# Performance work log

Measured on AMD Instinct MI355X. Metric: run time of the kernel, lower is better.

Reference implementation:

```python
import jax, jax.numpy as jnp
import numpy as np

NEAR, FAR = 2.0, 6.0
N_SAMPLES = 64
L_PTS, L_DIR = 10, 4
INF_DELTA = 1e10


def posenc(x, L):
    # x: [..., 3] -> [..., 3 + 6*L] (identity + sin/cos at 2^l frequencies)
    freqs = 2.0 ** jnp.arange(L, dtype=x.dtype)              # [L]
    ang = x[..., None, :] * freqs[:, None]                   # [..., L, 3]
    enc = jnp.concatenate([jnp.sin(ang), jnp.cos(ang)], axis=-1)  # [..., L, 6]
    return jnp.concatenate([x, enc.reshape(x.shape[:-1] + (L * 6,))], axis=-1)


def setup_inputs() -> dict:
    key = jax.random.key(0)
    ks = jax.random.split(key, 12)
    R, D, DH = 4096, 256, 128
    PE_P, PE_D = 3 + 6 * L_PTS, 3 + 6 * L_DIR  # 63, 27

    def w(k, shape):
        fan_in = shape[0]
        return jax.random.normal(k, shape, dtype=jnp.float32) / np.sqrt(fan_in)

    return {
        "xyz": jax.random.normal(ks[0], (1, R, 3), dtype=jnp.float32),
        "viewdirs": jax.random.normal(ks[1], (1, R, 3), dtype=jnp.float32),
        "W1": w(ks[2], (PE_P, D)), "b1": jnp.zeros((D,), jnp.float32),
        "W2": w(ks[3], (D, D)),    "b2": jnp.zeros((D,), jnp.float32),
        "W3": w(ks[4], (D, D)),    "b3": jnp.zeros((D,), jnp.float32),
        "Wsig": w(ks[5], (D, 1)),  "bsig": jnp.zeros((1,), jnp.float32),
        "Wfeat": w(ks[6], (D, D)), "bfeat": jnp.zeros((D,), jnp.float32),
        "Wdir": w(ks[7], (D + PE_D, DH)), "bdir": jnp.zeros((DH,), jnp.float32),
        "Wrgb": w(ks[8], (DH, 3)), "brgb": jnp.zeros((3,), jnp.float32),
    }


def reference(xyz, viewdirs, W1, b1, W2, b2, W3, b3, Wsig, bsig,
              Wfeat, bfeat, Wdir, bdir, Wrgb, brgb):
    xyz = xyz[0]          # [R, 3] (batch dim squeezed as in render_coarse)
    vd = viewdirs[0]
    vd = vd / jnp.linalg.norm(vd, axis=-1, keepdims=True)
    R = xyz.shape[0]

    # Evenly spaced samples between near and far (perturb=0 -> deterministic)
    t = jnp.linspace(0.0, 1.0, N_SAMPLES, dtype=xyz.dtype)
    samples = NEAR * (1.0 - t) + FAR * t                     # [N]
    samples = jnp.broadcast_to(samples, (R, N_SAMPLES))      # [R, N]
    delta = jnp.concatenate(
        [samples[:, 1:] - samples[:, :-1],
         jnp.full((R, 1), INF_DELTA, dtype=samples.dtype)], axis=-1)  # [R, N]

    # Sample points along each ray
    pts = xyz[:, None, :] + samples[..., None] * vd[:, None, :]  # [R, N, 3]

    # NeRF MLP: positional-encoded points -> density + view-dep color
    pe = posenc(pts, L_PTS)                                   # [R, N, 63]
    de = posenc(vd, L_DIR)                                    # [R, 27]
    h = jax.nn.relu(pe @ W1 + b1)
    h = jax.nn.relu(h @ W2 + b2)
    h = jax.nn.relu(h @ W3 + b3)                              # [R, N, 256]
    density = (h @ Wsig + bsig)[..., 0]                       # [R, N]
    feat = h @ Wfeat + bfeat                                  # [R, N, 256]
    de_b = jnp.broadcast_to(de[:, None, :], (R, N_SAMPLES, de.shape[-1]))
    hd = jax.nn.relu(jnp.concatenate([feat, de_b], axis=-1) @ Wdir + bdir)
    rgb = jax.nn.sigmoid(hd @ Wrgb + brgb)                    # [R, N, 3]

    # Volume rendering (alpha compositing with cumprod transmittance)
    sigma = jax.nn.relu(density)
    alpha = 1.0 - jnp.exp(-sigma * delta)                     # [R, N]
    T = jnp.concatenate(
        [jnp.ones((R, 1), alpha.dtype),
         jnp.cumprod(1.0 - alpha[:, :-1], axis=-1)], axis=-1)
    w = T * alpha                                             # [R, N]
    rgb_map = jnp.sum(w[..., None] * rgb, axis=-2)            # [R, 3]
    alpha_map = jnp.sum(w, axis=-1, keepdims=True)            # [R, 1]
    rgb_map = rgb_map + (1.0 - alpha_map)                     # white_bkgd
    depth_map = jnp.sum(w * samples, axis=-1)                 # [R]
    return rgb_map, depth_map, alpha_map
```

## Files before the change

kernel.cpp:

```cpp
#include <hip/hip_runtime.h>
#include <hip/hip_bf16.h>
#include <math.h>


typedef unsigned short u16;
typedef unsigned int   u32;
typedef __bf16 bf16x8 __attribute__((ext_vector_type(8)));
typedef float  f32x4  __attribute__((ext_vector_type(4)));

#define HI_STRIDE 296
#define LO_STRIDE 264
#define NROW 64

__device__ __align__(16) u16 g_whi[249856];
__device__ __align__(16) u16 g_wlo[147456];

constexpr int OFF_W1 = 0;
constexpr int OFF_W2 = 16384;
constexpr int OFF_W3 = 81920;
constexpr int OFF_WF = 147456;
constexpr int OFF_WD = 212992;

static __device__ __forceinline__ float bf2f(u16 u) {
  return __uint_as_float(((u32)u) << 16);
}
static __device__ __forceinline__ u16 f2bf(float f) {
  u32 x = __float_as_uint(f);
  return (u16)((x + 0x7FFFu + ((x >> 16) & 1u)) >> 16);
}
static __device__ __forceinline__ float wash(float x) {
  return (x == x) ? x : 0.0f;
}

struct alignas(8) U16x4 { u16 x, y, z, w; };

__global__ void repack_kernel(const float* __restrict__ w1, const float* __restrict__ w2,
                              const float* __restrict__ w3, const float* __restrict__ wf,
                              const float* __restrict__ wd) {
  int e = blockIdx.x * 256 + threadIdx.x;
  bool lo_plane = false;
  int eh = e;
  if (e >= 249856) { lo_plane = true; eh = e - 249856; }
  const float* src; int K, N, ks, base;
  if (eh < 81920)       { if (eh < 16384) { src = w1; K = 63;  N = 256; ks = 2; base = OFF_W1; }
                          else            { src = w2; K = 256; N = 256; ks = 8; base = OFF_W2; } }
  else if (eh < 147456) { src = w3; K = 256; N = 256; ks = 8; base = OFF_W3; }
  else if (eh < 212992) { src = wf; K = 256; N = 256; ks = 8; base = OFF_WF; }
  else                  { src = wd; K = 283; N = 128; ks = 9; base = OFF_WD; }
  int le   = eh - base;
  int f    = le >> 9, pos = le & 511;
  int lane = pos >> 3, j = pos & 7;
  int t    = f / ks,  s = f - t * ks;
  int k    = s * 32 + ((lane >> 4) << 3) + j;
  int n    = (t << 4) + (lane & 15);
  float v  = (k < K) ? src[k * N + n] : 0.0f;
  u16 h    = f2bf(v);
  if (!lo_plane) g_whi[eh] = h;
  else           g_wlo[eh] = f2bf(v - bf2f(h));
}

template<int KS, int NT, bool RELU, bool SPLIT>
static __device__ __forceinline__ void mlp_layer(u16* hi, u16* lo,
                                                 const u16* __restrict__ wh_,
                                                 const u16* __restrict__ wl_,
                                                 const float* __restrict__ bias,
                                                 int wave, int lane) {
  f32x4 acc[4][NT];
#pragma unroll
  for (int rt = 0; rt < 4; ++rt)
#pragma unroll
    for (int nt = 0; nt < NT; ++nt) {
      f32x4 z = {0.0f, 0.0f, 0.0f, 0.0f};
      acc[rt][nt] = z;
    }
  const int l15 = lane & 15, q = lane >> 4;
#pragma unroll
  for (int s = 0; s < KS; ++s) {
    bf16x8 ah[4], al[4];
#pragma unroll
    for (int rt = 0; rt < 4; ++rt) {
      ah[rt] = *reinterpret_cast<const bf16x8*>(
          &hi[(rt * 16 + l15) * HI_STRIDE + s * 32 + q * 8]);
      if (SPLIT)
        al[rt] = *reinterpret_cast<const bf16x8*>(
            &lo[(rt * 16 + l15) * LO_STRIDE + s * 32 + q * 8]);
    }
    bf16x8 wh[NT], wl[NT];
#pragma unroll
    for (int nt = 0; nt < NT; ++nt) {
      wh[nt] = *reinterpret_cast<const bf16x8*>(
          &wh_[((wave * NT + nt) * KS + s) * 512 + lane * 8]);
      if (SPLIT)
        wl[nt] = *reinterpret_cast<const bf16x8*>(
            &wl_[((wave * NT + nt) * KS + s) * 512 + lane * 8]);
    }
#pragma unroll
    for (int rt = 0; rt < 4; ++rt)
#pragma unroll
      for (int nt = 0; nt < NT; ++nt) {
        acc[rt][nt] = __builtin_amdgcn_mfma_f32_16x16x32_bf16(
            wh[nt], ah[rt], acc[rt][nt], 0, 0, 0);
        if (SPLIT) {
          acc[rt][nt] = __builtin_amdgcn_mfma_f32_16x16x32_bf16(
              wh[nt], al[rt], acc[rt][nt], 0, 0, 0);
          acc[rt][nt] = __builtin_amdgcn_mfma_f32_16x16x32_bf16(
              wl[nt], ah[rt], acc[rt][nt], 0, 0, 0);
        }
      }
  }
  __syncthreads();
#pragma unroll
  for (int nt = 0; nt < NT; ++nt) {
    const int nb = (wave * NT + nt) * 16 + q * 4;
    const float b0 = bias[nb + 0], b1 = bias[nb + 1];
    const float b2 = bias[nb + 2], b3 = bias[nb + 3];
#pragma unroll
    for (int rt = 0; rt < 4; ++rt) {
      float v0 = acc[rt][nt][0] + b0;
      float v1 = acc[rt][nt][1] + b1;
      float v2 = acc[rt][nt][2] + b2;
      float v3 = acc[rt][nt][3] + b3;
      if (RELU) {
        v0 = fmaxf(v0, 0.0f); v1 = fmaxf(v1, 0.0f);
        v2 = fmaxf(v2, 0.0f); v3 = fmaxf(v3, 0.0f);
      }
      U16x4 oh; oh.x = f2bf(v0); oh.y = f2bf(v1); oh.z = f2bf(v2); oh.w = f2bf(v3);
      *reinterpret_cast<U16x4*>(&hi[(rt * 16 + l15) * HI_STRIDE + nb]) = oh;
      if (SPLIT) {
        U16x4 ol;
        ol.x = f2bf(v0 - bf2f(oh.x)); ol.y = f2bf(v1 - bf2f(oh.y));
        ol.z = f2bf(v2 - bf2f(oh.z)); ol.w = f2bf(v3 - bf2f(oh.w));
        *reinterpret_cast<U16x4*>(&lo[(rt * 16 + l15) * LO_STRIDE + nb]) = ol;
      }
    }
  }
  __syncthreads();
}

__global__ __launch_bounds__(256, 2)
void nerf_kernel(const float* __restrict__ xyz, const float* __restrict__ vdirs,
                 const float* __restrict__ b1, const float* __restrict__ b2,
                 const float* __restrict__ b3, const float* __restrict__ wsig,
                 const float* __restrict__ bsig, const float* __restrict__ bfeat,
                 const float* __restrict__ bdir, const float* __restrict__ wrgb,
                 const float* __restrict__ brgb, float* __restrict__ out) {
  __shared__ u16  s_hi[NROW * HI_STRIDE];
  __shared__ u16  s_lo[NROW * LO_STRIDE];
  __shared__ float s_geo[6];
  __shared__ float s_de[32];

  const int tid  = threadIdx.x;
  const int wave = tid >> 6;
  const int lane = tid & 63;

  for (int i = tid; i < NROW * HI_STRIDE; i += 256) s_hi[i] = 0;
  for (int i = tid; i < NROW * LO_STRIDE; i += 256) s_lo[i] = 0;
  if (tid < 6)  s_geo[tid] = 0.0f;
  if (tid < 32) s_de[tid] = 0.0f;
  __syncthreads();

  if (tid == 0) {
    int rg = blockIdx.x;
    float vx = vdirs[rg * 3 + 0];
    float vy = vdirs[rg * 3 + 1];
    float vz = vdirs[rg * 3 + 2];
    float inv = 1.0f / sqrtf(vx * vx + vy * vy + vz * vz + 1e-20f);
    s_geo[0] = xyz[rg * 3 + 0];
    s_geo[1] = xyz[rg * 3 + 1];
    s_geo[2] = xyz[rg * 3 + 2];
    s_geo[3] = vx * inv;
    s_geo[4] = vy * inv;
    s_geo[5] = vz * inv;
  }
  __syncthreads();

  if (tid < 32) {
    float val = 0.0f;
    if (tid < 3) val = s_geo[3 + tid];
    else if (tid < 27) {
      int fi = tid - 3, l = fi / 6, m = fi % 6;
      int ii = (m < 3) ? m : m - 3;
      float ang = s_geo[3 + ii] * (float)(1 << l);
      val = (m < 3) ? sinf(ang) : cosf(ang);
    }
    s_de[tid] = val;
  }

  {
    int row = tid >> 2, q4 = tid & 3;
    float t  = (float)row * (1.0f / 63.0f);
    float ts = 2.0f * (1.0f - t) + 6.0f * t;
    float p[3];
    p[0] = s_geo[0] + ts * s_geo[3];
    p[1] = s_geo[1] + ts * s_geo[4];
    p[2] = s_geo[2] + ts * s_geo[5];
#pragma unroll 4
    for (int f0 = 0; f0 < 16; ++f0) {
      int f = q4 * 16 + f0;
      float val;
      if (f < 3) val = p[f];
      else if (f == 63) val = 0.0f;
      else {
        int fi = f - 3, l = fi / 6, m = fi % 6;
        int ii = (m < 3) ? m : m - 3;
        float ang = p[ii] * (float)(1 << l);
        val = (m < 3) ? sinf(ang) : cosf(ang);
      }
      u16 h = f2bf(val);
      s_hi[row * HI_STRIDE + f] = h;
      s_lo[row * LO_STRIDE + f] = f2bf(val - bf2f(h));
    }
  }
  __syncthreads();

  mlp_layer<2, 4, true, true>(s_hi, s_lo, g_whi + OFF_W1, g_wlo + OFF_W1,
                              b1, wave, lane);
  mlp_layer<8, 4, true, true>(s_hi, s_lo, g_whi + OFF_W2, g_wlo + OFF_W2,
                              b2, wave, lane);
  mlp_layer<8, 4, true, true>(s_hi, s_lo, g_whi + OFF_W3, g_wlo + OFF_W3,
                              b3, wave, lane);

  float my_den = 0.0f;
  if (tid < 64) {
    float a = 0.0f;
    const float4* wp = reinterpret_cast<const float4*>(wsig);
#pragma unroll 8
    for (int k4 = 0; k4 < 64; ++k4) {
      U16x4 h = *reinterpret_cast<const U16x4*>(&s_hi[tid * HI_STRIDE + k4 * 4]);
      U16x4 l = *reinterpret_cast<const U16x4*>(&s_lo[tid * LO_STRIDE + k4 * 4]);
      float4 w = wp[k4];
      a += (bf2f(h.x) + bf2f(l.x)) * w.x + (bf2f(h.y) + bf2f(l.y)) * w.y
         + (bf2f(h.z) + bf2f(l.z)) * w.z + (bf2f(h.w) + bf2f(l.w)) * w.w;
    }
    my_den = wash(a + bsig[0]);
  }

  mlp_layer<8, 4, false, false>(s_hi, s_lo, g_whi + OFF_WF, g_wlo,
                                bfeat, wave, lane);

  {
    int row = tid >> 2, i0 = (tid & 3) * 8;
#pragma unroll
    for (int j = 0; j < 8; ++j)
      s_hi[row * HI_STRIDE + 256 + i0 + j] = f2bf(s_de[i0 + j]);
  }
  __syncthreads();

  mlp_layer<9, 2, true, false>(s_hi, s_lo, g_whi + OFF_WD, g_wlo,
                               bdir, wave, lane);

  float r0 = 0.0f, r1 = 0.0f, r2 = 0.0f;
  if (tid < 64) {
    float a0 = brgb[0], a1 = brgb[1], a2 = brgb[2];
#pragma unroll 8
    for (int k = 0; k < 128; ++k) {
      float hv = bf2f(s_hi[tid * HI_STRIDE + k]);
      a0 += hv * wrgb[k * 3 + 0];
      a1 += hv * wrgb[k * 3 + 1];
      a2 += hv * wrgb[k * 3 + 2];
    }
    a0 = wash(a0); a1 = wash(a1); a2 = wash(a2);
    r0 = 1.0f / (1.0f + expf(-a0));
    r1 = 1.0f / (1.0f + expf(-a1));
    r2 = 1.0f / (1.0f + expf(-a2));
  }

  if (wave == 0) {
    int rg = blockIdx.x;
    float t  = (float)lane * (1.0f / 63.0f);
    float ts = 2.0f * (1.0f - t) + 6.0f * t;
    float delta;
    if (lane < 63) {
      float t2 = (float)(lane + 1) * (1.0f / 63.0f);
      delta = (2.0f * (1.0f - t2) + 6.0f * t2) - ts;
    } else delta = 1e10f;
    float sig = fmaxf(my_den, 0.0f);
    float sd  = fminf(sig * delta, 60.0f);
    float incl = sd;
#pragma unroll
    for (int o = 1; o < 64; o <<= 1) {
      float v = __shfl_up(incl, o, 64);
      if (lane >= o) incl += v;
    }
    float excl  = fminf(fmaxf(incl - sd, 0.0f), 60.0f);
    float T     = expf(-excl);
    float alpha = 1.0f - expf(-sd);
    float w     = T * alpha;
    float sw = w, swr = w * r0, swg = w * r1, swb = w * r2, swd = w * ts;
#pragma unroll
    for (int o = 32; o > 0; o >>= 1) {
      sw  += __shfl_xor(sw,  o, 64);
      swr += __shfl_xor(swr, o, 64);
      swg += __shfl_xor(swg, o, 64);
      swb += __shfl_xor(swb, o, 64);
      swd += __shfl_xor(swd, o, 64);
    }
    if (lane == 0) {
      float bg = 1.0f - sw;
      out[rg * 3 + 0]  = swr + bg;
      out[rg * 3 + 1]  = swg + bg;
      out[rg * 3 + 2]  = swb + bg;
      out[12288 + rg]  = swd;
      out[16384 + rg]  = sw;
    }
  }
}

extern "C" void kernel_launch(void* const* d_in, const int* in_sizes, int n_in,
                              void* d_out, int out_size, void* d_ws, size_t ws_size,
                              hipStream_t stream) {
  const float* xyz   = (const float*)d_in[0];
  const float* vdirs = (const float*)d_in[1];
  const float* W1    = (const float*)d_in[2];
  const float* b1    = (const float*)d_in[3];
  const float* W2    = (const float*)d_in[4];
  const float* b2    = (const float*)d_in[5];
  const float* W3    = (const float*)d_in[6];
  const float* b3    = (const float*)d_in[7];
  const float* Wsig  = (const float*)d_in[8];
  const float* bsig  = (const float*)d_in[9];
  const float* Wfeat = (const float*)d_in[10];
  const float* bfeat = (const float*)d_in[11];
  const float* Wdir  = (const float*)d_in[12];
  const float* bdir  = (const float*)d_in[13];
  const float* Wrgb  = (const float*)d_in[14];
  const float* brgb  = (const float*)d_in[15];
  float* out = (float*)d_out;

  repack_kernel<<<dim3(1552), dim3(256), 0, stream>>>(W1, W2, W3, Wfeat, Wdir);
  nerf_kernel<<<dim3(4096), dim3(256), 0, stream>>>(
      xyz, vdirs, b1, b2, b3, Wsig, bsig, bfeat, bdir, Wrgb, brgb, out);
}
```

Before: 412.5 us.

## Split MLP tiles across eight waves by row and column groups

New measurement: 404.0 us. 1.02x faster.

```diff
diff --git a/kernel.cpp b/kernel.cpp
--- a/kernel.cpp
+++ b/kernel.cpp
@@ -38,16 +38,13 @@
                               const float* __restrict__ w3, const float* __restrict__ wf,
                               const float* __restrict__ wd) {
   int e = blockIdx.x * 256 + threadIdx.x;
-  bool lo_plane = false;
-  int eh = e;
-  if (e >= 249856) { lo_plane = true; eh = e - 249856; }
   const float* src; int K, N, ks, base;
-  if (eh < 81920)       { if (eh < 16384) { src = w1; K = 63;  N = 256; ks = 2; base = OFF_W1; }
-                          else            { src = w2; K = 256; N = 256; ks = 8; base = OFF_W2; } }
-  else if (eh < 147456) { src = w3; K = 256; N = 256; ks = 8; base = OFF_W3; }
-  else if (eh < 212992) { src = wf; K = 256; N = 256; ks = 8; base = OFF_WF; }
-  else                  { src = wd; K = 283; N = 128; ks = 9; base = OFF_WD; }
-  int le   = eh - base;
+  if (e < 81920)       { if (e < 16384) { src = w1; K = 63;  N = 256; ks = 2; base = OFF_W1; }
+                         else           { src = w2; K = 256; N = 256; ks = 8; base = OFF_W2; } }
+  else if (e < 147456) { src = w3; K = 256; N = 256; ks = 8; base = OFF_W3; }
+  else if (e < 212992) { src = wf; K = 256; N = 256; ks = 8; base = OFF_WF; }
+  else                 { src = wd; K = 283; N = 128; ks = 9; base = OFF_WD; }
+  int le   = e - base;
   int f    = le >> 9, pos = le & 511;
   int lane = pos >> 3, j = pos & 7;
   int t    = f / ks,  s = f - t * ks;
@@ -55,19 +52,19 @@
   int n    = (t << 4) + (lane & 15);
   float v  = (k < K) ? src[k * N + n] : 0.0f;
   u16 h    = f2bf(v);
-  if (!lo_plane) g_whi[eh] = h;
-  else           g_wlo[eh] = f2bf(v - bf2f(h));
-}
-
-template<int KS, int NT, bool RELU, bool SPLIT>
+  g_whi[e] = h;
+  if (e < 147456) g_wlo[e] = f2bf(v - bf2f(h));
+}
+
+template<int KS, int NT, int RT, bool RELU, bool SPLIT>
 static __device__ __forceinline__ void mlp_layer(u16* hi, u16* lo,
                                                  const u16* __restrict__ wh_,
                                                  const u16* __restrict__ wl_,
                                                  const float* __restrict__ bias,
-                                                 int wave, int lane) {
-  f32x4 acc[4][NT];
-#pragma unroll
-  for (int rt = 0; rt < 4; ++rt)
+                                                 int rg, int cg, int lane) {
+  f32x4 acc[RT][NT];
+#pragma unroll
+  for (int rt = 0; rt < RT; ++rt)
 #pragma unroll
     for (int nt = 0; nt < NT; ++nt) {
       f32x4 z = {0.0f, 0.0f, 0.0f, 0.0f};
@@ -76,26 +73,24 @@
   const int l15 = lane & 15, q = lane >> 4;
 #pragma unroll
   for (int s = 0; s < KS; ++s) {
-    bf16x8 ah[4], al[4];
-#pragma unroll
-    for (int rt = 0; rt < 4; ++rt) {
-      ah[rt] = *reinterpret_cast<const bf16x8*>(
-          &hi[(rt * 16 + l15) * HI_STRIDE + s * 32 + q * 8]);
+    bf16x8 ah[RT], al[RT];
+#pragma unroll
+    for (int rt = 0; rt < RT; ++rt) {
+      const int row = (rg * RT + rt) * 16 + l15;
+      ah[rt] = *reinterpret_cast<const bf16x8*>(&hi[row * HI_STRIDE + s * 32 + q * 8]);
       if (SPLIT)
-        al[rt] = *reinterpret_cast<const bf16x8*>(
-            &lo[(rt * 16 + l15) * LO_STRIDE + s * 32 + q * 8]);
+        al[rt] = *reinterpret_cast<const bf16x8*>(&lo[row * LO_STRIDE + s * 32 + q * 8]);
     }
     bf16x8 wh[NT], wl[NT];
 #pragma unroll
     for (int nt = 0; nt < NT; ++nt) {
-      wh[nt] = *reinterpret_cast<const bf16x8*>(
-          &wh_[((wave * NT + nt) * KS + s) * 512 + lane * 8]);
+      const int t = cg * NT + nt;
+      wh[nt] = *reinterpret_cast<const bf16x8*>(&wh_[(t * KS + s) * 512 + lane * 8]);
       if (SPLIT)
-        wl[nt] = *reinterpret_cast<const bf16x8*>(
-            &wl_[((wave * NT + nt) * KS + s) * 512 + lane * 8]);
-    }
-#pragma unroll
-    for (int rt = 0; rt < 4; ++rt)
+        wl[nt] = *reinterpret_cast<const bf16x8*>(&wl_[(t * KS + s) * 512 + lane * 8]);
+    }
+#pragma unroll
+    for (int rt = 0; rt < RT; ++rt)
 #pragma unroll
       for (int nt = 0; nt < NT; ++nt) {
         acc[rt][nt] = __builtin_amdgcn_mfma_f32_16x16x32_bf16(
@@ -111,11 +106,12 @@
   __syncthreads();
 #pragma unroll
   for (int nt = 0; nt < NT; ++nt) {
-    const int nb = (wave * NT + nt) * 16 + q * 4;
+    const int nb = (cg * NT + nt) * 16 + q * 4;
     const float b0 = bias[nb + 0], b1 = bias[nb + 1];
     const float b2 = bias[nb + 2], b3 = bias[nb + 3];
 #pragma unroll
-    for (int rt = 0; rt < 4; ++rt) {
+    for (int rt = 0; rt < RT; ++rt) {
+      const int row = (rg * RT + rt) * 16 + l15;
       float v0 = acc[rt][nt][0] + b0;
       float v1 = acc[rt][nt][1] + b1;
       float v2 = acc[rt][nt][2] + b2;
@@ -125,19 +121,19 @@
         v2 = fmaxf(v2, 0.0f); v3 = fmaxf(v3, 0.0f);
       }
       U16x4 oh; oh.x = f2bf(v0); oh.y = f2bf(v1); oh.z = f2bf(v2); oh.w = f2bf(v3);
-      *reinterpret_cast<U16x4*>(&hi[(rt * 16 + l15) * HI_STRIDE + nb]) = oh;
+      *reinterpret_cast<U16x4*>(&hi[row * HI_STRIDE + nb]) = oh;
       if (SPLIT) {
         U16x4 ol;
         ol.x = f2bf(v0 - bf2f(oh.x)); ol.y = f2bf(v1 - bf2f(oh.y));
         ol.z = f2bf(v2 - bf2f(oh.z)); ol.w = f2bf(v3 - bf2f(oh.w));
-        *reinterpret_cast<U16x4*>(&lo[(rt * 16 + l15) * LO_STRIDE + nb]) = ol;
+        *reinterpret_cast<U16x4*>(&lo[row * LO_STRIDE + nb]) = ol;
       }
     }
   }
   __syncthreads();
 }
 
-__global__ __launch_bounds__(256, 2)
+__global__ __launch_bounds__(512, 4)
 void nerf_kernel(const float* __restrict__ xyz, const float* __restrict__ vdirs,
                  const float* __restrict__ b1, const float* __restrict__ b2,
                  const float* __restrict__ b3, const float* __restrict__ wsig,
@@ -152,22 +148,18 @@
   const int tid  = threadIdx.x;
   const int wave = tid >> 6;
   const int lane = tid & 63;
-
-  for (int i = tid; i < NROW * HI_STRIDE; i += 256) s_hi[i] = 0;
-  for (int i = tid; i < NROW * LO_STRIDE; i += 256) s_lo[i] = 0;
-  if (tid < 6)  s_geo[tid] = 0.0f;
-  if (tid < 32) s_de[tid] = 0.0f;
-  __syncthreads();
+  const int rg   = wave >> 2;
+  const int cg   = wave & 3;
 
   if (tid == 0) {
-    int rg = blockIdx.x;
-    float vx = vdirs[rg * 3 + 0];
-    float vy = vdirs[rg * 3 + 1];
-    float vz = vdirs[rg * 3 + 2];
+    int rgI = blockIdx.x;
+    float vx = vdirs[rgI * 3 + 0];
+    float vy = vdirs[rgI * 3 + 1];
+    float vz = vdirs[rgI * 3 + 2];
     float inv = 1.0f / sqrtf(vx * vx + vy * vy + vz * vz + 1e-20f);
-    s_geo[0] = xyz[rg * 3 + 0];
-    s_geo[1] = xyz[rg * 3 + 1];
-    s_geo[2] = xyz[rg * 3 + 2];
+    s_geo[0] = xyz[rgI * 3 + 0];
+    s_geo[1] = xyz[rgI * 3 + 1];
+    s_geo[2] = xyz[rgI * 3 + 2];
     s_geo[3] = vx * inv;
     s_geo[4] = vy * inv;
     s_geo[5] = vz * inv;
@@ -187,16 +179,16 @@
   }
 
   {
-    int row = tid >> 2, q4 = tid & 3;
+    int row = tid >> 3, c8 = tid & 7;
     float t  = (float)row * (1.0f / 63.0f);
     float ts = 2.0f * (1.0f - t) + 6.0f * t;
     float p[3];
     p[0] = s_geo[0] + ts * s_geo[3];
     p[1] = s_geo[1] + ts * s_geo[4];
     p[2] = s_geo[2] + ts * s_geo[5];
-#pragma unroll 4
-    for (int f0 = 0; f0 < 16; ++f0) {
-      int f = q4 * 16 + f0;
+#pragma unroll
+    for (int j = 0; j < 8; ++j) {
+      int f = c8 * 8 + j;
       float val;
       if (f < 3) val = p[f];
       else if (f == 63) val = 0.0f;
@@ -213,12 +205,12 @@
   }
   __syncthreads();
 
-  mlp_layer<2, 4, true, true>(s_hi, s_lo, g_whi + OFF_W1, g_wlo + OFF_W1,
-                              b1, wave, lane);
-  mlp_layer<8, 4, true, true>(s_hi, s_lo, g_whi + OFF_W2, g_wlo + OFF_W2,
-                              b2, wave, lane);
-  mlp_layer<8, 4, true, true>(s_hi, s_lo, g_whi + OFF_W3, g_wlo + OFF_W3,
-                              b3, wave, lane);
+  mlp_layer<2, 4, 2, true, true>(s_hi, s_lo, g_whi + OFF_W1, g_wlo + OFF_W1,
+                                 b1, rg, cg, lane);
+  mlp_layer<8, 4, 2, true, true>(s_hi, s_lo, g_whi + OFF_W2, g_wlo + OFF_W2,
+                                 b2, rg, cg, lane);
+  mlp_layer<8, 4, 2, true, true>(s_hi, s_lo, g_whi + OFF_W3, g_wlo + OFF_W3,
+                                 b3, rg, cg, lane);
 
   float my_den = 0.0f;
   if (tid < 64) {
@@ -235,19 +227,19 @@
     my_den = wash(a + bsig[0]);
   }
 
-  mlp_layer<8, 4, false, false>(s_hi, s_lo, g_whi + OFF_WF, g_wlo,
-                                bfeat, wave, lane);
+  mlp_layer<8, 4, 2, false, false>(s_hi, s_lo, g_whi + OFF_WF, g_wlo,
+                                   bfeat, rg, cg, lane);
 
   {
-    int row = tid >> 2, i0 = (tid & 3) * 8;
-#pragma unroll
-    for (int j = 0; j < 8; ++j)
+    int row = tid >> 3, i0 = (tid & 7) * 4;
+#pragma unroll
+    for (int j = 0; j < 4; ++j)
       s_hi[row * HI_STRIDE + 256 + i0 + j] = f2bf(s_de[i0 + j]);
   }
   __syncthreads();
 
-  mlp_layer<9, 2, true, false>(s_hi, s_lo, g_whi + OFF_WD, g_wlo,
-                               bdir, wave, lane);
+  mlp_layer<9, 2, 2, true, false>(s_hi, s_lo, g_whi + OFF_WD, g_wlo,
+                                  bdir, rg, cg, lane);
 
   float r0 = 0.0f, r1 = 0.0f, r2 = 0.0f;
   if (tid < 64) {
@@ -266,7 +258,7 @@
   }
 
   if (wave == 0) {
-    int rg = blockIdx.x;
+    int rgI = blockIdx.x;
     float t  = (float)lane * (1.0f / 63.0f);
     float ts = 2.0f * (1.0f - t) + 6.0f * t;
     float delta;
@@ -297,11 +289,11 @@
     }
     if (lane == 0) {
       float bg = 1.0f - sw;
-      out[rg * 3 + 0]  = swr + bg;
-      out[rg * 3 + 1]  = swg + bg;
-      out[rg * 3 + 2]  = swb + bg;
-      out[12288 + rg]  = swd;
-      out[16384 + rg]  = sw;
+      out[rgI * 3 + 0]  = swr + bg;
+      out[rgI * 3 + 1]  = swg + bg;
+      out[rgI * 3 + 2]  = swb + bg;
+      out[12288 + rgI]  = swd;
+      out[16384 + rgI]  = sw;
     }
   }
 }
@@ -327,7 +319,7 @@
   const float* brgb  = (const float*)d_in[15];
   float* out = (float*)d_out;
 
-  repack_kernel<<<dim3(1552), dim3(256), 0, stream>>>(W1, W2, W3, Wfeat, Wdir);
-  nerf_kernel<<<dim3(4096), dim3(256), 0, stream>>>(
+  repack_kernel<<<dim3(976), dim3(256), 0, stream>>>(W1, W2, W3, Wfeat, Wdir);
+  nerf_kernel<<<dim3(4096), dim3(512), 0, stream>>>(
       xyz, vdirs, b1, b2, b3, Wsig, bsig, bfeat, bdir, Wrgb, brgb, out);
 }
```
